# Performance work log

Measured on AMD Instinct MI355X. Metric: run time of the kernel, lower is better.

The kernel has to match this reference:

```python
import jax, jax.numpy as jnp
import numpy as np

MARGIN = 0.5
EPS = 1e-5


def setup_inputs() -> dict:
    key = jax.random.key(0)
    k1, k2 = jax.random.split(key)
    n, d, n_new, n_old = 8192, 256, 4096, 4096
    feature = jax.random.normal(k1, (n, d), dtype=jnp.float32)
    target = jax.random.randint(k2, (n,), 0, 100, dtype=jnp.int64)
    new_idx = jnp.arange(n_new, dtype=jnp.int64)
    old_idx = jnp.arange(n_old, dtype=jnp.int64)
    return {"feature": feature, "target": target, "new_idx": new_idx, "old_idx": old_idx}


def _triplet_loss(feature, target, new_idx, old_idx):
    n = feature.shape[0]
    n_new = new_idx.shape[0]
    # alpha switch is based on static shape, exactly as in the torch code
    alpha = 0.9 if old_idx.shape[0] != 0 else 0.5

    sim = feature @ feature.T                      # [n, n]
    sim_new = sim[:, new_idx]                      # [n, n_new]
    t_new = target[new_idx]                        # [n_new]

    same_new = target[:, None] == t_new[None, :]   # [n, n_new]
    is_new_row = jnp.arange(n) < n_new             # [n]

    # positive pairs (only defined for rows i < n_new)
    pos_mask = same_new & (sim_new < 1.0 - EPS)
    pos_loss_new = jnp.sum(jnp.where(pos_mask, 1.0 - sim_new, 0.0), axis=1)  # [n]
    # faithful to the torch bug: rows i >= n_new reuse the stale pos_pair_
    # from the last new row (i = n_new - 1)
    stale_pos = pos_loss_new[n_new - 1]
    pos_loss = jnp.where(is_new_row, pos_loss_new, stale_pos)

    # negatives: new rows scan all columns, old rows scan only new_idx columns
    diff_all = target[:, None] != target[None, :]
    neg_all = jnp.sum(jnp.where(diff_all & (sim > MARGIN), sim, 0.0), axis=1)
    neg_newcols = jnp.sum(jnp.where((~same_new) & (sim_new > MARGIN), sim_new, 0.0), axis=1)
    neg_loss = jnp.where(is_new_row, neg_all, neg_newcols)

    return jnp.mean(alpha * pos_loss + (1.0 - alpha) * neg_loss)


def reference(feature, target, new_idx, old_idx):
    return _triplet_loss(feature, target, new_idx, old_idx)
```

## Files before the change

kernel.cpp:

```cpp
#include <hip/hip_runtime.h>
#include <hip/hip_bf16.h>
#include <stdint.h>

#define MARGIN   0.5f
#define POS_THR  (1.0f - 1e-5f)

typedef __attribute__((ext_vector_type(8))) short  short8;
typedef __attribute__((ext_vector_type(4))) float  f32x4;

#define BM 128
#define BN 128
#define BK 32
#define NPANEL_SHIFT 7
#define NSLOTS 256

__device__ __forceinline__ ushort f2bf_rne(float x) {
  uint32_t u = __float_as_uint(x);
  u += 0x7fffu + ((u >> 16) & 1u);
  return (ushort)(u >> 16);
}

__device__ __forceinline__ void async_load16(const ushort* g, ushort* l) {
  __builtin_amdgcn_global_load_lds(
      (__attribute__((address_space(1))) void*)(const_cast<ushort*>(g)),
      (__attribute__((address_space(3))) void*)(l),
      16, 0, 0);
}

__global__ void prep_kernel(const float* __restrict__ src, ushort* __restrict__ dst,
                            int* __restrict__ cnt, int* __restrict__ flags,
                            float* __restrict__ misc, int total8, int n, int npanel) {
  int i = blockIdx.x * blockDim.x + threadIdx.x;
  if (i < total8) {
    const float4* s4 = reinterpret_cast<const float4*>(src);
    float4 a = s4[i * 2], b = s4[i * 2 + 1];
    short8 o;
    o[0] = (short)f2bf_rne(a.x); o[1] = (short)f2bf_rne(a.y);
    o[2] = (short)f2bf_rne(a.z); o[3] = (short)f2bf_rne(a.w);
    o[4] = (short)f2bf_rne(b.x); o[5] = (short)f2bf_rne(b.y);
    o[6] = (short)f2bf_rne(b.z); o[7] = (short)f2bf_rne(b.w);
    reinterpret_cast<short8*>(dst)[i] = o;
  }
  if (i < n) cnt[i] = 0;
  if (i < npanel) flags[i] = 0;
  if (i < NSLOTS + 1) misc[i] = 0.f;
}

__global__ void count_kernel(const int* __restrict__ new_idx, int* __restrict__ cnt,
                             int* __restrict__ flags, int n_new) {
  int i = blockIdx.x * blockDim.x + threadIdx.x;
  if (i < n_new) {
    int idx = new_idx[i];
    atomicAdd(&cnt[idx], 1);
    atomicOr(&flags[idx >> NPANEL_SHIFT], 1);
  }
}

__global__ __launch_bounds__(256) void simloss_kernel(
    const ushort* __restrict__ fb, const int* __restrict__ target,
    const int* __restrict__ cnt, const int* __restrict__ colHasNew,
    float* __restrict__ misc, int d, int n_new, float alpha) {
  __shared__ __align__(16) ushort Als[3][BM * BK];
  __shared__ __align__(16) ushort Bls[3][BN * BK];
  __shared__ int   t_row[BM];
  __shared__ int   t_col[BN];
  __shared__ float cw_col[BN];
  __shared__ float red[4];

  const int tid = threadIdx.x;
  const int rowBase = blockIdx.y * BM;
  const int colBase = blockIdx.x * BN;

  if (rowBase >= n_new && colHasNew[blockIdx.x] == 0) return;

  if (tid < BM) t_row[tid] = target[rowBase + tid];
  if (tid < BN) {
    t_col[tid]  = target[colBase + tid];
    cw_col[tid] = (float)cnt[colBase + tid];
  }

  const int lane = tid & 63;
  const int wid  = tid >> 6;
  const int wr   = wid >> 1;
  const int wc   = wid & 1;
  const int l15  = lane & 15;
  const int kb   = lane >> 4;

  const int ch0 = (wid * 2 + 0) * 64 + lane;
  const int ch1 = (wid * 2 + 1) * 64 + lane;
  const int r0 = ch0 >> 2, kq0 = (ch0 & 3) ^ ((ch0 >> 3) & 3);
  const int r1 = ch1 >> 2, kq1 = (ch1 & 3) ^ ((ch1 >> 3) & 3);
  const ushort* gA0 = fb + (size_t)(rowBase + r0) * d + kq0 * 8;
  const ushort* gA1 = fb + (size_t)(rowBase + r1) * d + kq1 * 8;
  const ushort* gB0 = fb + (size_t)(colBase + r0) * d + kq0 * 8;
  const ushort* gB1 = fb + (size_t)(colBase + r1) * d + kq1 * 8;
  const int lo0 = (wid * 2 + 0) * 512;
  const int lo1 = (wid * 2 + 1) * 512;

  f32x4 acc[4][4] = {};

  int aoff[4], boff[4];
#pragma unroll
  for (int m = 0; m < 4; ++m) {
    int row = wr * 64 + m * 16 + l15;
    aoff[m] = row * 32 + ((kb ^ ((row >> 1) & 3)) * 8);
  }
#pragma unroll
  for (int nf = 0; nf < 4; ++nf) {
    int row = wc * 64 + nf * 16 + l15;
    boff[nf] = row * 32 + ((kb ^ ((row >> 1) & 3)) * 8);
  }

  asm volatile("s_waitcnt vmcnt(0) lgkmcnt(0)" ::: "memory");

  async_load16(gA0, &Als[0][lo0]);
  async_load16(gA1, &Als[0][lo1]);
  async_load16(gB0, &Bls[0][lo0]);
  async_load16(gB1, &Bls[0][lo1]);
  const int nk = d / BK;
  if (nk > 1) {
    async_load16(gA0 + BK, &Als[1][lo0]);
    async_load16(gA1 + BK, &Als[1][lo1]);
    async_load16(gB0 + BK, &Bls[1][lo0]);
    async_load16(gB1 + BK, &Bls[1][lo1]);
  }

  int cur = 0;
  for (int t = 0; t < nk; ++t) {
    if (t == nk - 1) asm volatile("s_waitcnt vmcnt(0)" ::: "memory");
    else             asm volatile("s_waitcnt vmcnt(4)" ::: "memory");
    asm volatile("s_barrier" ::: "memory");

    if (t + 2 < nk) {
      int nxt = cur + 2; if (nxt >= 3) nxt -= 3;
      int ko = (t + 2) * BK;
      async_load16(gA0 + ko, &Als[nxt][lo0]);
      async_load16(gA1 + ko, &Als[nxt][lo1]);
      async_load16(gB0 + ko, &Bls[nxt][lo0]);
      async_load16(gB1 + ko, &Bls[nxt][lo1]);
    }

    short8 afr[4], bfr[4];
#pragma unroll
    for (int m = 0; m < 4; ++m)
      afr[m] = *reinterpret_cast<const short8*>(&Als[cur][aoff[m]]);
#pragma unroll
    for (int nf = 0; nf < 4; ++nf)
      bfr[nf] = *reinterpret_cast<const short8*>(&Bls[cur][boff[nf]]);

#pragma unroll
    for (int m = 0; m < 4; ++m)
#pragma unroll
      for (int nf = 0; nf < 4; ++nf)
        acc[m][nf] = __builtin_amdgcn_mfma_f32_16x16x32_bf16(bfr[nf], afr[m], acc[m][nf], 0, 0, 0);

    cur = (cur + 1 == 3) ? 0 : cur + 1;
  }

  const float beta = 1.0f - alpha;
  int tc_r[4][4]; float cw_r[4][4];
#pragma unroll
  for (int nf = 0; nf < 4; ++nf)
#pragma unroll
    for (int q = 0; q < 4; ++q) {
      int cl = wc * 64 + nf * 16 + kb * 4 + q;
      tc_r[nf][q] = t_col[cl];
      cw_r[nf][q] = cw_col[cl];
    }

  const int  stale_row = n_new - 1;
  const bool blk_stale = (stale_row >= rowBase) && (stale_row < rowBase + BM);
  const int  srl = stale_row - rowBase;

  float c = 0.f;
#pragma unroll
  for (int m = 0; m < 4; ++m) {
    int rl = wr * 64 + m * 16 + l15;
    int r  = rowBase + rl;
    int tr = t_row[rl];
    bool isnew = (r < n_new);
    float p = 0.f, ng = 0.f;
#pragma unroll
    for (int nf = 0; nf < 4; ++nf)
#pragma unroll
      for (int q = 0; q < 4; ++q) {
        float s = acc[m][nf][q];
        bool same = (tr == tc_r[nf][q]);
        if (isnew) {
          if (same && s < POS_THR)  p  += cw_r[nf][q] * (1.0f - s);
          if (!same && s > MARGIN)  ng += s;
        } else {
          if (!same && s > MARGIN)  ng += cw_r[nf][q] * s;
        }
      }
    if (blk_stale && wr == (srl >> 6) && m == ((srl >> 4) & 3)) {
      float pr = p;
      pr += __shfl_xor(pr, 16); pr += __shfl_xor(pr, 32);
      if (lane < 16 && rl == srl) atomicAdd(&misc[NSLOTS], pr);
    }
    c += isnew ? fmaf(alpha, p, beta * ng) : beta * ng;
  }
#pragma unroll
  for (int off = 32; off; off >>= 1) c += __shfl_xor(c, off);
  if (lane == 0) red[wid] = c;
  __syncthreads();
  if (tid == 0)
    atomicAdd(&misc[(blockIdx.y * gridDim.x + blockIdx.x) & (NSLOTS - 1)],
              red[0] + red[1] + red[2] + red[3]);
}

__global__ void finalize_kernel(const float* __restrict__ misc,
                                float* __restrict__ out, int n, int n_new,
                                float alpha) {
  int t = threadIdx.x;
  float c = misc[t] + misc[t + 64] + misc[t + 128] + misc[t + 192];
#pragma unroll
  for (int off = 32; off; off >>= 1) c += __shfl_xor(c, off);
  if (t == 0)
    out[0] = (c + (float)(n - n_new) * alpha * misc[NSLOTS]) / (float)n;
}

extern "C" void kernel_launch(void* const* d_in, const int* in_sizes, int n_in,
                              void* d_out, int out_size, void* d_ws, size_t ws_size,
                              hipStream_t stream) {
  const float* feature = (const float*)d_in[0];
  const int*   target  = (const int*)d_in[1];
  const int*   new_idx = (const int*)d_in[2];

  const int n     = in_sizes[1];
  const int d     = in_sizes[0] / n;
  const int n_new = in_sizes[2];
  const int n_old = (n_in > 3) ? in_sizes[3] : 0;
  const float alpha = (n_old != 0) ? 0.9f : 0.5f;
  const int npanel = n / BN;

  auto al = [](size_t x) { return (x + 255) & ~(size_t)255; };
  char* ws = (char*)d_ws;
  ushort* fb    = (ushort*)ws;
  size_t  off   = al((size_t)n * d * sizeof(ushort));
  int*    cnt   = (int*)(ws + off);   off += al((size_t)n * sizeof(int));
  int*    flags = (int*)(ws + off);   off += al((size_t)npanel * sizeof(int));
  float*  misc  = (float*)(ws + off);

  int total8 = (n * d) / 8;
  prep_kernel<<<(total8 + 255) / 256, 256, 0, stream>>>(feature, fb, cnt, flags,
                                                        misc, total8, n, npanel);
  count_kernel<<<(n_new + 255) / 256, 256, 0, stream>>>(new_idx, cnt, flags, n_new);

  dim3 grid(n / BN, n / BM);
  simloss_kernel<<<grid, 256, 0, stream>>>(fb, target, cnt, flags, misc,
                                           d, n_new, alpha);

  finalize_kernel<<<1, 64, 0, stream>>>(misc, (float*)d_out, n, n_new, alpha);
}
```

Measured before the change: 152.6 us.

## Merge count and finalize kernels into prep and simloss launches

Folds the new_idx histogram into an extra block of the prep kernel, using a shared-memory histogram instead of global atomics. The separate finalize kernel is replaced by a last-block-done reduction inside simloss, guarded by a global counter. This cuts the pipeline from four launches to two, removing launch and inter-kernel gaps. It also adds sched_barrier and explicit lgkmcnt waits in the MFMA loop. The risks are that the histogram runs in a single block, and every block now does a fence plus an atomic at exit, including skipped ones.

```diff
diff --git a/kernel.cpp b/kernel.cpp
--- a/kernel.cpp
+++ b/kernel.cpp
@@ -13,6 +13,7 @@
 #define BK 32
 #define NPANEL_SHIFT 7
 #define NSLOTS 256
+#define MAXN_HIST 8192
 
 __device__ __forceinline__ ushort f2bf_rne(float x) {
   uint32_t u = __float_as_uint(x);
@@ -28,196 +29,224 @@
 }
 
 __global__ void prep_kernel(const float* __restrict__ src, ushort* __restrict__ dst,
+                            const int* __restrict__ new_idx,
                             int* __restrict__ cnt, int* __restrict__ flags,
-                            float* __restrict__ misc, int total8, int n, int npanel) {
-  int i = blockIdx.x * blockDim.x + threadIdx.x;
-  if (i < total8) {
-    const float4* s4 = reinterpret_cast<const float4*>(src);
-    float4 a = s4[i * 2], b = s4[i * 2 + 1];
-    short8 o;
-    o[0] = (short)f2bf_rne(a.x); o[1] = (short)f2bf_rne(a.y);
-    o[2] = (short)f2bf_rne(a.z); o[3] = (short)f2bf_rne(a.w);
-    o[4] = (short)f2bf_rne(b.x); o[5] = (short)f2bf_rne(b.y);
-    o[6] = (short)f2bf_rne(b.z); o[7] = (short)f2bf_rne(b.w);
-    reinterpret_cast<short8*>(dst)[i] = o;
-  }
-  if (i < n) cnt[i] = 0;
-  if (i < npanel) flags[i] = 0;
-  if (i < NSLOTS + 1) misc[i] = 0.f;
-}
-
-__global__ void count_kernel(const int* __restrict__ new_idx, int* __restrict__ cnt,
-                             int* __restrict__ flags, int n_new) {
-  int i = blockIdx.x * blockDim.x + threadIdx.x;
-  if (i < n_new) {
-    int idx = new_idx[i];
-    atomicAdd(&cnt[idx], 1);
-    atomicOr(&flags[idx >> NPANEL_SHIFT], 1);
-  }
+                            float* __restrict__ misc, int* __restrict__ done,
+                            int total8, int n, int npanel, int n_new, int convBlocks) {
+  __shared__ int hcnt[MAXN_HIST];
+  __shared__ int hflag[MAXN_HIST / BN];
+  const int tid = threadIdx.x;
+  if ((int)blockIdx.x < convBlocks) {
+    int i = blockIdx.x * blockDim.x + tid;
+    if (i < total8) {
+      const float4* s4 = reinterpret_cast<const float4*>(src);
+      float4 a = s4[i * 2], b = s4[i * 2 + 1];
+      short8 o;
+      o[0] = (short)f2bf_rne(a.x); o[1] = (short)f2bf_rne(a.y);
+      o[2] = (short)f2bf_rne(a.z); o[3] = (short)f2bf_rne(a.w);
+      o[4] = (short)f2bf_rne(b.x); o[5] = (short)f2bf_rne(b.y);
+      o[6] = (short)f2bf_rne(b.z); o[7] = (short)f2bf_rne(b.w);
+      reinterpret_cast<short8*>(dst)[i] = o;
+    }
+    return;
+  }
+  for (int i = tid; i < n; i += blockDim.x) hcnt[i] = 0;
+  for (int i = tid; i < npanel; i += blockDim.x) hflag[i] = 0;
+  __syncthreads();
+  for (int i = tid; i < n_new; i += blockDim.x) atomicAdd(&hcnt[new_idx[i]], 1);
+  __syncthreads();
+  for (int i = tid; i < n; i += blockDim.x) {
+    int c = hcnt[i];
+    cnt[i] = c;
+    if (c) atomicOr(&hflag[i >> NPANEL_SHIFT], 1);
+  }
+  __syncthreads();
+  for (int i = tid; i < npanel; i += blockDim.x) flags[i] = hflag[i];
+  for (int i = tid; i < NSLOTS + 1; i += blockDim.x) misc[i] = 0.f;
+  if (tid == 0) *done = 0;
 }
 
 __global__ __launch_bounds__(256) void simloss_kernel(
     const ushort* __restrict__ fb, const int* __restrict__ target,
     const int* __restrict__ cnt, const int* __restrict__ colHasNew,
-    float* __restrict__ misc, int d, int n_new, float alpha) {
+    float* __restrict__ misc, int* __restrict__ done, float* __restrict__ out,
+    int d, int n, int n_new, float alpha) {
   __shared__ __align__(16) ushort Als[3][BM * BK];
   __shared__ __align__(16) ushort Bls[3][BN * BK];
   __shared__ int   t_row[BM];
   __shared__ int   t_col[BN];
   __shared__ float cw_col[BN];
   __shared__ float red[4];
+  __shared__ int   lastFlag;
 
   const int tid = threadIdx.x;
   const int rowBase = blockIdx.y * BM;
   const int colBase = blockIdx.x * BN;
-
-  if (rowBase >= n_new && colHasNew[blockIdx.x] == 0) return;
-
-  if (tid < BM) t_row[tid] = target[rowBase + tid];
-  if (tid < BN) {
-    t_col[tid]  = target[colBase + tid];
-    cw_col[tid] = (float)cnt[colBase + tid];
-  }
-
   const int lane = tid & 63;
   const int wid  = tid >> 6;
-  const int wr   = wid >> 1;
-  const int wc   = wid & 1;
-  const int l15  = lane & 15;
-  const int kb   = lane >> 4;
-
-  const int ch0 = (wid * 2 + 0) * 64 + lane;
-  const int ch1 = (wid * 2 + 1) * 64 + lane;
-  const int r0 = ch0 >> 2, kq0 = (ch0 & 3) ^ ((ch0 >> 3) & 3);
-  const int r1 = ch1 >> 2, kq1 = (ch1 & 3) ^ ((ch1 >> 3) & 3);
-  const ushort* gA0 = fb + (size_t)(rowBase + r0) * d + kq0 * 8;
-  const ushort* gA1 = fb + (size_t)(rowBase + r1) * d + kq1 * 8;
-  const ushort* gB0 = fb + (size_t)(colBase + r0) * d + kq0 * 8;
-  const ushort* gB1 = fb + (size_t)(colBase + r1) * d + kq1 * 8;
-  const int lo0 = (wid * 2 + 0) * 512;
-  const int lo1 = (wid * 2 + 1) * 512;
-
-  f32x4 acc[4][4] = {};
-
-  int aoff[4], boff[4];
-#pragma unroll
-  for (int m = 0; m < 4; ++m) {
-    int row = wr * 64 + m * 16 + l15;
-    aoff[m] = row * 32 + ((kb ^ ((row >> 1) & 3)) * 8);
-  }
-#pragma unroll
-  for (int nf = 0; nf < 4; ++nf) {
-    int row = wc * 64 + nf * 16 + l15;
-    boff[nf] = row * 32 + ((kb ^ ((row >> 1) & 3)) * 8);
-  }
-
-  asm volatile("s_waitcnt vmcnt(0) lgkmcnt(0)" ::: "memory");
-
-  async_load16(gA0, &Als[0][lo0]);
-  async_load16(gA1, &Als[0][lo1]);
-  async_load16(gB0, &Bls[0][lo0]);
-  async_load16(gB1, &Bls[0][lo1]);
-  const int nk = d / BK;
-  if (nk > 1) {
-    async_load16(gA0 + BK, &Als[1][lo0]);
-    async_load16(gA1 + BK, &Als[1][lo1]);
-    async_load16(gB0 + BK, &Bls[1][lo0]);
-    async_load16(gB1 + BK, &Bls[1][lo1]);
-  }
-
-  int cur = 0;
-  for (int t = 0; t < nk; ++t) {
-    if (t == nk - 1) asm volatile("s_waitcnt vmcnt(0)" ::: "memory");
-    else             asm volatile("s_waitcnt vmcnt(4)" ::: "memory");
-    asm volatile("s_barrier" ::: "memory");
-
-    if (t + 2 < nk) {
-      int nxt = cur + 2; if (nxt >= 3) nxt -= 3;
-      int ko = (t + 2) * BK;
-      async_load16(gA0 + ko, &Als[nxt][lo0]);
-      async_load16(gA1 + ko, &Als[nxt][lo1]);
-      async_load16(gB0 + ko, &Bls[nxt][lo0]);
-      async_load16(gB1 + ko, &Bls[nxt][lo1]);
-    }
-
-    short8 afr[4], bfr[4];
-#pragma unroll
-    for (int m = 0; m < 4; ++m)
-      afr[m] = *reinterpret_cast<const short8*>(&Als[cur][aoff[m]]);
+
+  const bool skip = (rowBase >= n_new) && (colHasNew[blockIdx.x] == 0);
+
+  if (!skip) {
+    if (tid < BM) t_row[tid] = target[rowBase + tid];
+    if (tid < BN) {
+      t_col[tid]  = target[colBase + tid];
+      cw_col[tid] = (float)cnt[colBase + tid];
+    }
+
+    const int wr  = wid >> 1;
+    const int wc  = wid & 1;
+    const int l15 = lane & 15;
+    const int kb  = lane >> 4;
+
+    const int ch0 = (wid * 2 + 0) * 64 + lane;
+    const int ch1 = (wid * 2 + 1) * 64 + lane;
+    const int r0 = ch0 >> 2, kq0 = (ch0 & 3) ^ ((ch0 >> 3) & 3);
+    const int r1 = ch1 >> 2, kq1 = (ch1 & 3) ^ ((ch1 >> 3) & 3);
+    const ushort* gA0 = fb + (size_t)(rowBase + r0) * d + kq0 * 8;
+    const ushort* gA1 = fb + (size_t)(rowBase + r1) * d + kq1 * 8;
+    const ushort* gB0 = fb + (size_t)(colBase + r0) * d + kq0 * 8;
+    const ushort* gB1 = fb + (size_t)(colBase + r1) * d + kq1 * 8;
+    const int lo0 = (wid * 2 + 0) * 512;
+    const int lo1 = (wid * 2 + 1) * 512;
+
+    f32x4 acc[4][4] = {};
+
+    int aoff[4], boff[4];
+#pragma unroll
+    for (int m = 0; m < 4; ++m) {
+      int row = wr * 64 + m * 16 + l15;
+      aoff[m] = row * 32 + ((kb ^ ((row >> 1) & 3)) * 8);
+    }
+#pragma unroll
+    for (int nf = 0; nf < 4; ++nf) {
+      int row = wc * 64 + nf * 16 + l15;
+      boff[nf] = row * 32 + ((kb ^ ((row >> 1) & 3)) * 8);
+    }
+
+    asm volatile("s_waitcnt vmcnt(0) lgkmcnt(0)" ::: "memory");
+    __builtin_amdgcn_sched_barrier(0);
+
+    async_load16(gA0, &Als[0][lo0]);
+    async_load16(gA1, &Als[0][lo1]);
+    async_load16(gB0, &Bls[0][lo0]);
+    async_load16(gB1, &Bls[0][lo1]);
+    const int nk = d / BK;
+    if (nk > 1) {
+      async_load16(gA0 + BK, &Als[1][lo0]);
+      async_load16(gA1 + BK, &Als[1][lo1]);
+      async_load16(gB0 + BK, &Bls[1][lo0]);
+      async_load16(gB1 + BK, &Bls[1][lo1]);
+    }
+
+    int cur = 0;
+    for (int t = 0; t < nk; ++t) {
+      if (t == nk - 1) asm volatile("s_waitcnt vmcnt(0)" ::: "memory");
+      else             asm volatile("s_waitcnt vmcnt(4)" ::: "memory");
+      __builtin_amdgcn_s_barrier();
+      __builtin_amdgcn_sched_barrier(0);
+
+      if (t + 2 < nk) {
+        int nxt = cur + 2; if (nxt >= 3) nxt -= 3;
+        int ko = (t + 2) * BK;
+        async_load16(gA0 + ko, &Als[nxt][lo0]);
+        async_load16(gA1 + ko, &Als[nxt][lo1]);
+        async_load16(gB0 + ko, &Bls[nxt][lo0]);
+        async_load16(gB1 + ko, &Bls[nxt][lo1]);
+      }
+
+      short8 afr[4], bfr[4];
+#pragma unroll
+      for (int m = 0; m < 4; ++m)
+        afr[m] = *reinterpret_cast<const short8*>(&Als[cur][aoff[m]]);
+#pragma unroll
+      for (int nf = 0; nf < 4; ++nf)
+        bfr[nf] = *reinterpret_cast<const short8*>(&Bls[cur][boff[nf]]);
+      asm volatile("s_waitcnt lgkmcnt(0)" ::: "memory");
+      __builtin_amdgcn_sched_barrier(0);
+
+#pragma unroll
+      for (int m = 0; m < 4; ++m)
+#pragma unroll
+        for (int nf = 0; nf < 4; ++nf)
+          acc[m][nf] = __builtin_amdgcn_mfma_f32_16x16x32_bf16(bfr[nf], afr[m], acc[m][nf], 0, 0, 0);
+
+      cur = (cur + 1 == 3) ? 0 : cur + 1;
+    }
+
+    const float beta = 1.0f - alpha;
+    const int wr2 = wid >> 1, wc2 = wid & 1, l15b = lane & 15, kb2 = lane >> 4;
+    int tc_r[4][4]; float cw_r[4][4];
 #pragma unroll
     for (int nf = 0; nf < 4; ++nf)
-      bfr[nf] = *reinterpret_cast<const short8*>(&Bls[cur][boff[nf]]);
-
-#pragma unroll
-    for (int m = 0; m < 4; ++m)
+#pragma unroll
+      for (int q = 0; q < 4; ++q) {
+        int cl = wc2 * 64 + nf * 16 + kb2 * 4 + q;
+        tc_r[nf][q] = t_col[cl];
+        cw_r[nf][q] = cw_col[cl];
+      }
+
+    const int  stale_row = n_new - 1;
+    const bool blk_stale = (stale_row >= rowBase) && (stale_row < rowBase + BM);
+    const int  srl = stale_row - rowBase;
+
+    float c = 0.f;
+#pragma unroll
+    for (int m = 0; m < 4; ++m) {
+      int rl = wr2 * 64 + m * 16 + l15b;
+      int r  = rowBase + rl;
+      int tr = t_row[rl];
+      bool isnew = (r < n_new);
+      float p = 0.f, ng = 0.f;
 #pragma unroll
       for (int nf = 0; nf < 4; ++nf)
-        acc[m][nf] = __builtin_amdgcn_mfma_f32_16x16x32_bf16(bfr[nf], afr[m], acc[m][nf], 0, 0, 0);
-
-    cur = (cur + 1 == 3) ? 0 : cur + 1;
-  }
-
-  const float beta = 1.0f - alpha;
-  int tc_r[4][4]; float cw_r[4][4];
-#pragma unroll
-  for (int nf = 0; nf < 4; ++nf)
-#pragma unroll
-    for (int q = 0; q < 4; ++q) {
-      int cl = wc * 64 + nf * 16 + kb * 4 + q;
-      tc_r[nf][q] = t_col[cl];
-      cw_r[nf][q] = cw_col[cl];
-    }
-
-  const int  stale_row = n_new - 1;
-  const bool blk_stale = (stale_row >= rowBase) && (stale_row < rowBase + BM);
-  const int  srl = stale_row - rowBase;
-
-  float c = 0.f;
-#pragma unroll
-  for (int m = 0; m < 4; ++m) {
-    int rl = wr * 64 + m * 16 + l15;
-    int r  = rowBase + rl;
-    int tr = t_row[rl];
-    bool isnew = (r < n_new);
-    float p = 0.f, ng = 0.f;
-#pragma unroll
-    for (int nf = 0; nf < 4; ++nf)
-#pragma unroll
-      for (int q = 0; q < 4; ++q) {
-        float s = acc[m][nf][q];
-        bool same = (tr == tc_r[nf][q]);
-        if (isnew) {
-          if (same && s < POS_THR)  p  += cw_r[nf][q] * (1.0f - s);
-          if (!same && s > MARGIN)  ng += s;
-        } else {
-          if (!same && s > MARGIN)  ng += cw_r[nf][q] * s;
+#pragma unroll
+        for (int q = 0; q < 4; ++q) {
+          float s = acc[m][nf][q];
+          bool same = (tr == tc_r[nf][q]);
+          if (isnew) {
+            if (same && s < POS_THR)  p  += cw_r[nf][q] * (1.0f - s);
+            if (!same && s > MARGIN)  ng += s;
+          } else {
+            if (!same && s > MARGIN)  ng += cw_r[nf][q] * s;
+          }
         }
+      if (blk_stale && wr2 == (srl >> 6) && m == ((srl >> 4) & 3)) {
+        float pr = p;
+        pr += __shfl_xor(pr, 16); pr += __shfl_xor(pr, 32);
+        if (lane < 16 && rl == srl) atomicAdd(&misc[NSLOTS], pr);
       }
-    if (blk_stale && wr == (srl >> 6) && m == ((srl >> 4) & 3)) {
-      float pr = p;
-      pr += __shfl_xor(pr, 16); pr += __shfl_xor(pr, 32);
-      if (lane < 16 && rl == srl) atomicAdd(&misc[NSLOTS], pr);
-    }
-    c += isnew ? fmaf(alpha, p, beta * ng) : beta * ng;
-  }
-#pragma unroll
-  for (int off = 32; off; off >>= 1) c += __shfl_xor(c, off);
-  if (lane == 0) red[wid] = c;
-  __syncthreads();
-  if (tid == 0)
-    atomicAdd(&misc[(blockIdx.y * gridDim.x + blockIdx.x) & (NSLOTS - 1)],
-              red[0] + red[1] + red[2] + red[3]);
-}
-
-__global__ void finalize_kernel(const float* __restrict__ misc,
-                                float* __restrict__ out, int n, int n_new,
-                                float alpha) {
-  int t = threadIdx.x;
-  float c = misc[t] + misc[t + 64] + misc[t + 128] + misc[t + 192];
-#pragma unroll
-  for (int off = 32; off; off >>= 1) c += __shfl_xor(c, off);
-  if (t == 0)
-    out[0] = (c + (float)(n - n_new) * alpha * misc[NSLOTS]) / (float)n;
+      c += isnew ? fmaf(alpha, p, beta * ng) : beta * ng;
+    }
+#pragma unroll
+    for (int off = 32; off; off >>= 1) c += __shfl_xor(c, off);
+    if (lane == 0) red[wid] = c;
+    __syncthreads();
+    if (tid == 0)
+      atomicAdd(&misc[(blockIdx.y * gridDim.x + blockIdx.x) & (NSLOTS - 1)],
+                red[0] + red[1] + red[2] + red[3]);
+  }
+
+  __threadfence();
+  const int nblk = gridDim.x * gridDim.y;
+  if (tid == 0) lastFlag = (atomicAdd(done, 1) == nblk - 1) ? 1 : 0;
+  __syncthreads();
+  if (lastFlag) {
+    __threadfence();
+    float c = (tid < NSLOTS)
+        ? __hip_atomic_load(&misc[tid], __ATOMIC_RELAXED, __HIP_MEMORY_SCOPE_AGENT)
+        : 0.f;
+#pragma unroll
+    for (int off = 32; off; off >>= 1) c += __shfl_xor(c, off);
+    if (lane == 0) red[wid] = c;
+    __syncthreads();
+    if (tid == 0) {
+      float stale = __hip_atomic_load(&misc[NSLOTS], __ATOMIC_RELAXED,
+                                      __HIP_MEMORY_SCOPE_AGENT);
+      out[0] = (red[0] + red[1] + red[2] + red[3] +
+                (float)(n - n_new) * alpha * stale) / (float)n;
+    }
+  }
 }
 
 extern "C" void kernel_launch(void* const* d_in, const int* in_sizes, int n_in,
@@ -240,16 +269,16 @@
   size_t  off   = al((size_t)n * d * sizeof(ushort));
   int*    cnt   = (int*)(ws + off);   off += al((size_t)n * sizeof(int));
   int*    flags = (int*)(ws + off);   off += al((size_t)npanel * sizeof(int));
-  float*  misc  = (float*)(ws + off);
+  float*  misc  = (float*)(ws + off); off += al((size_t)(NSLOTS + 1) * sizeof(float));
+  int*    done  = (int*)(ws + off);
 
   int total8 = (n * d) / 8;
-  prep_kernel<<<(total8 + 255) / 256, 256, 0, stream>>>(feature, fb, cnt, flags,
-                                                        misc, total8, n, npanel);
-  count_kernel<<<(n_new + 255) / 256, 256, 0, stream>>>(new_idx, cnt, flags, n_new);
+  int convBlocks = (total8 + 255) / 256;
+  prep_kernel<<<convBlocks + 1, 256, 0, stream>>>(feature, fb, new_idx, cnt, flags,
+                                                  misc, done, total8, n, npanel,
+                                                  n_new, convBlocks);
 
   dim3 grid(n / BN, n / BM);
-  simloss_kernel<<<grid, 256, 0, stream>>>(fb, target, cnt, flags, misc,
-                                           d, n_new, alpha);
-
-  finalize_kernel<<<1, 64, 0, stream>>>(misc, (float*)d_out, n, n_new, alpha);
-}
+  simloss_kernel<<<grid, 256, 0, stream>>>(fb, target, cnt, flags, misc, done,
+                                           (float*)d_out, d, n, n_new, alpha);
+}
```

Result: slower. 401.1 us (+162.9%).

## Exploit Gram symmetry to compute only lower-triangular tiles; fuse count into prep

Applied to the files above, without the earlier changes.

The similarity matrix is symmetric, so only tiles with bx <= by are computed. Each off-diagonal tile also accumulates the transposed contribution, using per-row counts and a column-is-new mask, which roughly halves the MFMA work. The separate count kernel is merged into the prep kernel as one extra block that builds the histogram in shared memory, removing a launch. The change also adds explicit sched_barrier and lgkmcnt waits in the main loop. In exchange the epilogue does more per-element work, and the single histogram block serialises the count step.

```diff
diff --git a/kernel.cpp b/kernel.cpp
--- a/kernel.cpp
+++ b/kernel.cpp
@@ -13,6 +13,7 @@
 #define BK 32
 #define NPANEL_SHIFT 7
 #define NSLOTS 256
+#define MAXN_HIST 8192
 
 __device__ __forceinline__ ushort f2bf_rne(float x) {
   uint32_t u = __float_as_uint(x);
@@ -28,52 +29,68 @@
 }
 
 __global__ void prep_kernel(const float* __restrict__ src, ushort* __restrict__ dst,
+                            const int* __restrict__ new_idx,
                             int* __restrict__ cnt, int* __restrict__ flags,
-                            float* __restrict__ misc, int total8, int n, int npanel) {
-  int i = blockIdx.x * blockDim.x + threadIdx.x;
-  if (i < total8) {
-    const float4* s4 = reinterpret_cast<const float4*>(src);
-    float4 a = s4[i * 2], b = s4[i * 2 + 1];
-    short8 o;
-    o[0] = (short)f2bf_rne(a.x); o[1] = (short)f2bf_rne(a.y);
-    o[2] = (short)f2bf_rne(a.z); o[3] = (short)f2bf_rne(a.w);
-    o[4] = (short)f2bf_rne(b.x); o[5] = (short)f2bf_rne(b.y);
-    o[6] = (short)f2bf_rne(b.z); o[7] = (short)f2bf_rne(b.w);
-    reinterpret_cast<short8*>(dst)[i] = o;
-  }
-  if (i < n) cnt[i] = 0;
-  if (i < npanel) flags[i] = 0;
-  if (i < NSLOTS + 1) misc[i] = 0.f;
-}
-
-__global__ void count_kernel(const int* __restrict__ new_idx, int* __restrict__ cnt,
-                             int* __restrict__ flags, int n_new) {
-  int i = blockIdx.x * blockDim.x + threadIdx.x;
-  if (i < n_new) {
-    int idx = new_idx[i];
-    atomicAdd(&cnt[idx], 1);
-    atomicOr(&flags[idx >> NPANEL_SHIFT], 1);
-  }
+                            float* __restrict__ misc,
+                            int total8, int n, int npanel, int n_new, int convBlocks) {
+  __shared__ int hcnt[MAXN_HIST];
+  __shared__ int hflag[MAXN_HIST / BN];
+  const int tid = threadIdx.x;
+  if ((int)blockIdx.x < convBlocks) {
+    int i = blockIdx.x * blockDim.x + tid;
+    if (i < total8) {
+      const float4* s4 = reinterpret_cast<const float4*>(src);
+      float4 a = s4[i * 2], b = s4[i * 2 + 1];
+      short8 o;
+      o[0] = (short)f2bf_rne(a.x); o[1] = (short)f2bf_rne(a.y);
+      o[2] = (short)f2bf_rne(a.z); o[3] = (short)f2bf_rne(a.w);
+      o[4] = (short)f2bf_rne(b.x); o[5] = (short)f2bf_rne(b.y);
+      o[6] = (short)f2bf_rne(b.z); o[7] = (short)f2bf_rne(b.w);
+      reinterpret_cast<short8*>(dst)[i] = o;
+    }
+    return;
+  }
+  for (int i = tid; i < n; i += blockDim.x) hcnt[i] = 0;
+  for (int i = tid; i < npanel; i += blockDim.x) hflag[i] = 0;
+  __syncthreads();
+  for (int i = tid; i < n_new; i += blockDim.x) atomicAdd(&hcnt[new_idx[i]], 1);
+  __syncthreads();
+  for (int i = tid; i < n; i += blockDim.x) {
+    int c = hcnt[i];
+    cnt[i] = c;
+    if (c) atomicOr(&hflag[i >> NPANEL_SHIFT], 1);
+  }
+  __syncthreads();
+  for (int i = tid; i < npanel; i += blockDim.x) flags[i] = hflag[i];
+  for (int i = tid; i < NSLOTS + 1; i += blockDim.x) misc[i] = 0.f;
 }
 
 __global__ __launch_bounds__(256) void simloss_kernel(
     const ushort* __restrict__ fb, const int* __restrict__ target,
-    const int* __restrict__ cnt, const int* __restrict__ colHasNew,
+    const int* __restrict__ cnt, const int* __restrict__ flags,
     float* __restrict__ misc, int d, int n_new, float alpha) {
   __shared__ __align__(16) ushort Als[3][BM * BK];
   __shared__ __align__(16) ushort Bls[3][BN * BK];
   __shared__ int   t_row[BM];
   __shared__ int   t_col[BN];
   __shared__ float cw_col[BN];
+  __shared__ float cw_row[BM];
   __shared__ float red[4];
 
+  const int bx = blockIdx.x, by = blockIdx.y;
+  if (bx > by) return;
   const int tid = threadIdx.x;
-  const int rowBase = blockIdx.y * BM;
-  const int colBase = blockIdx.x * BN;
-
-  if (rowBase >= n_new && colHasNew[blockIdx.x] == 0) return;
-
-  if (tid < BM) t_row[tid] = target[rowBase + tid];
+  const int rowBase = by * BM;
+  const int colBase = bx * BN;
+  const bool diag = (bx == by);
+
+  if ((rowBase >= n_new && flags[bx] == 0) &&
+      (colBase >= n_new && flags[by] == 0)) return;
+
+  if (tid < BM) {
+    t_row[tid]  = target[rowBase + tid];
+    cw_row[tid] = (float)cnt[rowBase + tid];
+  }
   if (tid < BN) {
     t_col[tid]  = target[colBase + tid];
     cw_col[tid] = (float)cnt[colBase + tid];
@@ -112,6 +129,7 @@
   }
 
   asm volatile("s_waitcnt vmcnt(0) lgkmcnt(0)" ::: "memory");
+  __builtin_amdgcn_sched_barrier(0);
 
   async_load16(gA0, &Als[0][lo0]);
   async_load16(gA1, &Als[0][lo1]);
@@ -129,7 +147,8 @@
   for (int t = 0; t < nk; ++t) {
     if (t == nk - 1) asm volatile("s_waitcnt vmcnt(0)" ::: "memory");
     else             asm volatile("s_waitcnt vmcnt(4)" ::: "memory");
-    asm volatile("s_barrier" ::: "memory");
+    __builtin_amdgcn_s_barrier();
+    __builtin_amdgcn_sched_barrier(0);
 
     if (t + 2 < nk) {
       int nxt = cur + 2; if (nxt >= 3) nxt -= 3;
@@ -147,6 +166,8 @@
 #pragma unroll
     for (int nf = 0; nf < 4; ++nf)
       bfr[nf] = *reinterpret_cast<const short8*>(&Bls[cur][boff[nf]]);
+    asm volatile("s_waitcnt lgkmcnt(0)" ::: "memory");
+    __builtin_amdgcn_sched_barrier(0);
 
 #pragma unroll
     for (int m = 0; m < 4; ++m)
@@ -158,39 +179,51 @@
   }
 
   const float beta = 1.0f - alpha;
-  int tc_r[4][4]; float cw_r[4][4];
+  int tc_r[4][4]; float cw_c[4][4]; bool cn_r[4][4];
 #pragma unroll
   for (int nf = 0; nf < 4; ++nf)
 #pragma unroll
     for (int q = 0; q < 4; ++q) {
       int cl = wc * 64 + nf * 16 + kb * 4 + q;
       tc_r[nf][q] = t_col[cl];
-      cw_r[nf][q] = cw_col[cl];
+      cw_c[nf][q] = cw_col[cl];
+      cn_r[nf][q] = (colBase + cl) < n_new;
     }
 
   const int  stale_row = n_new - 1;
   const bool blk_stale = (stale_row >= rowBase) && (stale_row < rowBase + BM);
   const int  srl = stale_row - rowBase;
 
-  float c = 0.f;
+  float tot = 0.f;
 #pragma unroll
   for (int m = 0; m < 4; ++m) {
     int rl = wr * 64 + m * 16 + l15;
     int r  = rowBase + rl;
     int tr = t_row[rl];
-    bool isnew = (r < n_new);
-    float p = 0.f, ng = 0.f;
+    bool rnew = (r < n_new);
+    float cwr  = cw_row[rl];
+    float acwr = alpha * cwr;
+    float bcwr = beta * cwr;
+    float p = 0.f, ng = 0.f, t2 = 0.f;
 #pragma unroll
     for (int nf = 0; nf < 4; ++nf)
 #pragma unroll
       for (int q = 0; q < 4; ++q) {
         float s = acc[m][nf][q];
         bool same = (tr == tc_r[nf][q]);
-        if (isnew) {
-          if (same && s < POS_THR)  p  += cw_r[nf][q] * (1.0f - s);
-          if (!same && s > MARGIN)  ng += s;
+        bool gm = (s > MARGIN);
+        bool lp = (s < POS_THR);
+        if (rnew) {
+          if (same && lp) p  += cw_c[nf][q] * (1.0f - s);
+          if (!same && gm) ng += s;
         } else {
-          if (!same && s > MARGIN)  ng += cw_r[nf][q] * s;
+          if (!same && gm) ng += cw_c[nf][q] * s;
+        }
+        if (cn_r[nf][q]) {
+          if (same && lp)  t2 += acwr * (1.0f - s);
+          if (!same && gm) t2 += beta * s;
+        } else {
+          if (!same && gm) t2 += bcwr * s;
         }
       }
     if (blk_stale && wr == (srl >> 6) && m == ((srl >> 4) & 3)) {
@@ -198,14 +231,15 @@
       pr += __shfl_xor(pr, 16); pr += __shfl_xor(pr, 32);
       if (lane < 16 && rl == srl) atomicAdd(&misc[NSLOTS], pr);
     }
-    c += isnew ? fmaf(alpha, p, beta * ng) : beta * ng;
-  }
-#pragma unroll
-  for (int off = 32; off; off >>= 1) c += __shfl_xor(c, off);
-  if (lane == 0) red[wid] = c;
+    tot += rnew ? fmaf(alpha, p, beta * ng) : beta * ng;
+    if (!diag) tot += t2;
+  }
+#pragma unroll
+  for (int off = 32; off; off >>= 1) tot += __shfl_xor(tot, off);
+  if (lane == 0) red[wid] = tot;
   __syncthreads();
   if (tid == 0)
-    atomicAdd(&misc[(blockIdx.y * gridDim.x + blockIdx.x) & (NSLOTS - 1)],
+    atomicAdd(&misc[(by * gridDim.x + bx) & (NSLOTS - 1)],
               red[0] + red[1] + red[2] + red[3]);
 }
 
@@ -243,9 +277,10 @@
   float*  misc  = (float*)(ws + off);
 
   int total8 = (n * d) / 8;
-  prep_kernel<<<(total8 + 255) / 256, 256, 0, stream>>>(feature, fb, cnt, flags,
-                                                        misc, total8, n, npanel);
-  count_kernel<<<(n_new + 255) / 256, 256, 0, stream>>>(new_idx, cnt, flags, n_new);
+  int convBlocks = (total8 + 255) / 256;
+  prep_kernel<<<convBlocks + 1, 256, 0, stream>>>(feature, fb, new_idx, cnt, flags,
+                                                  misc, total8, n, npanel,
+                                                  n_new, convBlocks);
 
   dim3 grid(n / BN, n / BM);
   simloss_kernel<<<grid, 256, 0, stream>>>(fb, target, cnt, flags, misc,
```

Result: faster. 125.8 us (-17.6%).
